# Optimization experiments

Hardware: AMD Instinct MI355X
Metric: run time of the kernel (lower is better)

Reference implementation:

```python
import jax, jax.numpy as jnp
import numpy as np

TOP_K = 2


def setup_inputs() -> dict:
    key = jax.random.key(0)
    ks = jax.random.split(key, 5)
    B, S, H, E, F = 2, 4096, 2048, 8, 4096
    scale_h = 1.0 / np.sqrt(H)
    scale_f = 1.0 / np.sqrt(F)
    return {
        "hidden_states": jax.random.normal(ks[0], (B, S, H), jnp.float32),
        "gate_w": jax.random.normal(ks[1], (E, H), jnp.float32) * scale_h,
        "w1": jax.random.normal(ks[2], (E, F, H), jnp.float32) * scale_h,
        "w3": jax.random.normal(ks[3], (E, F, H), jnp.float32) * scale_h,
        "w2": jax.random.normal(ks[4], (E, H, F), jnp.float32) * scale_f,
    }


def reference(hidden_states, gate_w, w1, w3, w2):
    B, S, H = hidden_states.shape
    E = gate_w.shape[0]
    x = hidden_states.reshape(-1, H)                      # [T, H]
    T = x.shape[0]

    # Router: logits -> softmax(fp32) -> top-k -> renormalize
    router_logits = x @ gate_w.T                          # [T, E]
    probs = jax.nn.softmax(router_logits.astype(jnp.float32), axis=-1)
    topk_w, topk_idx = jax.lax.top_k(probs, TOP_K)        # [T, k]
    topk_w = topk_w / jnp.sum(topk_w, axis=-1, keepdims=True)
    topk_w = topk_w.astype(x.dtype)

    # Per-expert combine weight (0 for unselected experts) [T, E]
    combine = jnp.sum(jax.nn.one_hot(topk_idx, E, dtype=x.dtype)
                      * topk_w[..., None], axis=1)

    # Expert SwiGLU MLPs, weighted-accumulated (loop over fixed E=8)
    out = jnp.zeros((T, H), dtype=x.dtype)
    for e in range(E):
        h = jax.nn.silu(x @ w1[e].T) * (x @ w3[e].T)      # [T, F]
        out = out + (h @ w2[e].T) * combine[:, e:e + 1]   # [T, H]

    return out.reshape(B, S, H), router_logits
```

## Files before the change

### kernel.cpp

```cpp
#include <hip/hip_runtime.h>
#include <math.h>

#define T_TOK 8192
#define H_DIM 2048
#define F_DIM 4096
#define E_NUM 8
#define MAXPAIR (T_TOK * 2)
#define MAX_MT 136
#define BM 128
#define BN 128
#define BK 32
#define NCONV 2048

typedef __attribute__((ext_vector_type(4))) float f32x4;
typedef __attribute__((ext_vector_type(8))) short s16x8;
typedef __attribute__((ext_vector_type(8))) __bf16 bf16x8;
typedef __attribute__((ext_vector_type(4))) unsigned short u16x4;

__device__ __forceinline__ unsigned short f2bf(float f) {
  unsigned int u = __float_as_uint(f);
  u += 0x7FFFu + ((u >> 16) & 1u);
  return (unsigned short)(u >> 16);
}

__device__ __forceinline__ s16x8 pack8(f32x4 a, f32x4 b) {
  s16x8 r;
  r[0] = (short)f2bf(a.x); r[1] = (short)f2bf(a.y);
  r[2] = (short)f2bf(a.z); r[3] = (short)f2bf(a.w);
  r[4] = (short)f2bf(b.x); r[5] = (short)f2bf(b.y);
  r[6] = (short)f2bf(b.z); r[7] = (short)f2bf(b.w);
  return r;
}

#define GLD16(gsrc, ldst)                                                      \
  __builtin_amdgcn_global_load_lds(                                            \
      (__attribute__((address_space(1))) void*)(gsrc),                         \
      (__attribute__((address_space(3))) void*)(ldst), 16, 0, 0)

__global__ __launch_bounds__(256) void convert_kernel(
    const float* __restrict__ src, unsigned short* __restrict__ dst,
    long long n8) {
  long long i = (long long)blockIdx.x * 256 + threadIdx.x;
  const long long stride = (long long)gridDim.x * 256;
  for (; i < n8; i += stride) {
    f32x4 a = *(const f32x4*)(src + i * 8);
    f32x4 b = *(const f32x4*)(src + i * 8 + 4);
    *(s16x8*)(dst + i * 8) = pack8(a, b);
  }
}

__global__ __launch_bounds__(256) void router_kernel(
    const float* __restrict__ x, const float* __restrict__ gw,
    float* __restrict__ logits, unsigned short* __restrict__ xb,
    int* __restrict__ ctrl, int* __restrict__ tIdx, float* __restrict__ tW) {
  const int wid = threadIdx.x >> 6, lane = threadIdx.x & 63;
  const int t = blockIdx.x * 4 + wid;
  const float* xr = x + (size_t)t * H_DIM;
  float acc[E_NUM];
#pragma unroll
  for (int e = 0; e < E_NUM; ++e) acc[e] = 0.f;
#pragma unroll
  for (int c = 0; c < H_DIM / 256; ++c) {
    const int h0 = c * 256 + lane * 4;
    f32x4 xv = *(const f32x4*)(xr + h0);
    u16x4 p;
    p.x = f2bf(xv.x); p.y = f2bf(xv.y); p.z = f2bf(xv.z); p.w = f2bf(xv.w);
    *(u16x4*)(xb + (size_t)t * H_DIM + h0) = p;
#pragma unroll
    for (int e = 0; e < E_NUM; ++e) {
      f32x4 gv = *(const f32x4*)(gw + (size_t)e * H_DIM + h0);
      acc[e] += xv.x * gv.x + xv.y * gv.y + xv.z * gv.z + xv.w * gv.w;
    }
  }
#pragma unroll
  for (int e = 0; e < E_NUM; ++e) {
#pragma unroll
    for (int off = 32; off >= 1; off >>= 1) acc[e] += __shfl_xor(acc[e], off, 64);
  }
  if (lane == 0) {
#pragma unroll
    for (int e = 0; e < E_NUM; ++e) logits[(size_t)t * E_NUM + e] = acc[e];
    int i0 = 0;
    float m0 = acc[0];
    for (int e = 1; e < E_NUM; ++e)
      if (acc[e] > m0) { m0 = acc[e]; i0 = e; }
    int i1 = -1;
    float m1 = -3.4e38f;
    for (int e = 0; e < E_NUM; ++e)
      if (e != i0 && acc[e] > m1) { m1 = acc[e]; i1 = e; }
    float ex = expf(m1 - m0);
    float w0 = 1.f / (1.f + ex);
    float w1 = ex * w0;
    tIdx[t * 2] = i0; tIdx[t * 2 + 1] = i1;
    tW[t * 2] = w0;  tW[t * 2 + 1] = w1;
    atomicAdd(&ctrl[i0], 1);
    atomicAdd(&ctrl[i1], 1);
  }
}

__global__ __launch_bounds__(256) void plan_kernel(int* __restrict__ ctrl) {
  __shared__ int cnt[E_NUM], offs[E_NUM + 1], tbase[E_NUM + 1];
  const int t = threadIdx.x;
  if (t < E_NUM) cnt[t] = ctrl[t];
  __syncthreads();
  if (t == 0) {
    int off = 0, mt = 0;
    for (int e = 0; e < E_NUM; ++e) {
      offs[e] = off; tbase[e] = mt;
      ctrl[8 + e] = off;
      ctrl[16 + e] = off;
      off += cnt[e];
      mt += (cnt[e] + BM - 1) / BM;
    }
    offs[E_NUM] = off; tbase[E_NUM] = mt;
    ctrl[24] = mt;
  }
  __syncthreads();
  const int total = tbase[E_NUM];
  for (int i = t; i < total; i += 256) {
    int e = 0;
    while (tbase[e + 1] <= i) ++e;
    ctrl[32 + i] = e;
    ctrl[32 + MAX_MT + i] = offs[e] + (i - tbase[e]) * BM;
  }
}

__global__ __launch_bounds__(256) void scatter_kernel(
    const int* __restrict__ tIdx, const float* __restrict__ tW,
    int* __restrict__ ctrl, int* __restrict__ pairTok,
    float* __restrict__ pairWgt) {
  const int t = blockIdx.x * 256 + threadIdx.x;
  if (t >= T_TOK) return;
#pragma unroll
  for (int j = 0; j < 2; ++j) {
    const int e = tIdx[t * 2 + j];
    const int pos = atomicAdd(&ctrl[16 + e], 1);
    pairTok[pos] = t;
    pairWgt[pos] = tW[t * 2 + j];
  }
}

template <int BBF>
__global__ __launch_bounds__(256, 2) void gemm1_kernel(
    const float* __restrict__ w1f, const float* __restrict__ w3f,
    const unsigned short* __restrict__ w1b,
    const unsigned short* __restrict__ w3b,
    const unsigned short* __restrict__ xb, const int* __restrict__ ctrl,
    const int* __restrict__ pairTok, unsigned short* __restrict__ hbuf,
    const float* __restrict__ w2f, unsigned short* __restrict__ w2b,
    int nconv) {
  int gid = blockIdx.x;
  const int nconv3 = nconv * 3;
  if (gid < nconv3) {
    if ((gid % 3) == 2) {
      const int cid = gid / 3;
      const long long per = (long long)E_NUM * F_DIM * H_DIM / 8 / NCONV;
      long long i = (long long)cid * per + threadIdx.x;
      const long long end = (long long)(cid + 1) * per;
      for (; i < end; i += 256) {
        f32x4 a = *(const f32x4*)(w2f + i * 8);
        f32x4 b = *(const f32x4*)(w2f + i * 8 + 4);
        *(s16x8*)(w2b + i * 8) = pack8(a, b);
      }
      return;
    }
    gid = gid - (gid + 1) / 3;
  } else {
    gid = gid - nconv;
  }

  const int mtTotal = ctrl[24];
  const int mt = gid >> 5;
  const int nt = gid & 31;
  if (mt >= mtTotal) return;
  const int e = ctrl[32 + mt];
  const int mbase = ctrl[32 + MAX_MT + mt];
  int mValid = ctrl[8 + e] + ctrl[e] - mbase;
  if (mValid > BM) mValid = BM;
  const int nbase = nt * BN;

  __shared__ __align__(16) short sA[3][BM * BK];
  __shared__ __align__(16) short sB1[3][BM * BK];
  __shared__ __align__(16) short sB3[3][BM * BK];
  __shared__ int sTok[BM];

  const int tid = threadIdx.x;
  if (tid < BM) sTok[tid] = pairTok[mbase + (tid < mValid ? tid : 0)];
  __syncthreads();

  const int c0 = tid, c1 = tid + 256;
  const int r0 = c0 >> 2, r1 = c1 >> 2;
  const int kg0 = (c0 & 3) ^ ((r0 >> 1) & 3);
  const int kg1 = (c1 & 3) ^ ((r1 >> 1) & 3);

  const unsigned short* srcA0 = xb + (size_t)sTok[r0] * H_DIM + kg0 * 8;
  const unsigned short* srcA1 = xb + (size_t)sTok[r1] * H_DIM + kg1 * 8;
  const size_t wbase = (size_t)e * F_DIM * H_DIM;
  const float *f10, *f11, *f30, *f31;
  const unsigned short *p10, *p11, *p30, *p31;
  if constexpr (BBF) {
    p10 = w1b + wbase + (size_t)(nbase + r0) * H_DIM + kg0 * 8;
    p11 = w1b + wbase + (size_t)(nbase + r1) * H_DIM + kg1 * 8;
    p30 = w3b + wbase + (size_t)(nbase + r0) * H_DIM + kg0 * 8;
    p31 = w3b + wbase + (size_t)(nbase + r1) * H_DIM + kg1 * 8;
  } else {
    f10 = w1f + wbase + (size_t)(nbase + r0) * H_DIM + kg0 * 8;
    f11 = w1f + wbase + (size_t)(nbase + r1) * H_DIM + kg1 * 8;
    f30 = w3f + wbase + (size_t)(nbase + r0) * H_DIM + kg0 * 8;
    f31 = w3f + wbase + (size_t)(nbase + r1) * H_DIM + kg1 * 8;
  }

  f32x4 acc1[4][4], acc3[4][4];
  const f32x4 fz = {0.f, 0.f, 0.f, 0.f};
#pragma unroll
  for (int i = 0; i < 4; ++i)
#pragma unroll
    for (int j = 0; j < 4; ++j) { acc1[i][j] = fz; acc3[i][j] = fz; }

  const int lane = tid & 63, wid = tid >> 6;
  const int wm = (wid >> 1) * 64, wn = (wid & 1) * 64;
  const int rl = lane & 15, kq = lane >> 4;

  int aIdx[4], bIdx[4];
#pragma unroll
  for (int i = 0; i < 4; ++i) {
    const int ra = wm + i * 16 + rl;
    aIdx[i] = ra * BK + ((kq ^ ((ra >> 1) & 3)) * 8);
    const int rb = wn + i * 16 + rl;
    bIdx[i] = rb * BK + ((kq ^ ((rb >> 1) & 3)) * 8);
  }

#define STAGE1(buf, k0)                                                        \
  {                                                                            \
    GLD16(srcA0 + (k0), &sA[buf][c0 * 8]);                                     \
    GLD16(srcA1 + (k0), &sA[buf][c1 * 8]);                                     \
    if constexpr (BBF) {                                                       \
      GLD16(p10 + (k0), &sB1[buf][c0 * 8]);                                    \
      GLD16(p11 + (k0), &sB1[buf][c1 * 8]);                                    \
      GLD16(p30 + (k0), &sB3[buf][c0 * 8]);                                    \
      GLD16(p31 + (k0), &sB3[buf][c1 * 8]);                                    \
    } else {                                                                   \
      f32x4 t0 = *(const f32x4*)(f10 + (k0));                                  \
      f32x4 t1 = *(const f32x4*)(f10 + (k0) + 4);                              \
      *(s16x8*)&sB1[buf][c0 * 8] = pack8(t0, t1);                              \
      t0 = *(const f32x4*)(f11 + (k0));                                        \
      t1 = *(const f32x4*)(f11 + (k0) + 4);                                    \
      *(s16x8*)&sB1[buf][c1 * 8] = pack8(t0, t1);                              \
      t0 = *(const f32x4*)(f30 + (k0));                                        \
      t1 = *(const f32x4*)(f30 + (k0) + 4);                                    \
      *(s16x8*)&sB3[buf][c0 * 8] = pack8(t0, t1);                              \
      t0 = *(const f32x4*)(f31 + (k0));                                        \
      t1 = *(const f32x4*)(f31 + (k0) + 4);                                    \
      *(s16x8*)&sB3[buf][c1 * 8] = pack8(t0, t1);                              \
    }                                                                          \
  }

  STAGE1(0, 0);
  STAGE1(1, BK);

  const int NS = H_DIM / BK;
  int cur = 0;
  for (int s = 0; s < NS; ++s) {
    if (s + 2 < NS) {
      const int nxt = (cur + 2 >= 3) ? cur - 1 : cur + 2;
      STAGE1(nxt, (s + 2) * BK);
      if constexpr (BBF)
        asm volatile("s_waitcnt vmcnt(12)" ::: "memory");
      else
        asm volatile("s_waitcnt vmcnt(0) lgkmcnt(0)" ::: "memory");
    } else if (s + 2 == NS) {
      if constexpr (BBF)
        asm volatile("s_waitcnt vmcnt(6)" ::: "memory");
      else
        asm volatile("s_waitcnt vmcnt(0) lgkmcnt(0)" ::: "memory");
    } else {
      asm volatile("s_waitcnt vmcnt(0) lgkmcnt(0)" ::: "memory");
    }
    __builtin_amdgcn_s_barrier();
    asm volatile("" ::: "memory");

    bf16x8 af[4], bf1[4], bf3[4];
#pragma unroll
    for (int i = 0; i < 4; ++i) {
      af[i] = *(const bf16x8*)&sA[cur][aIdx[i]];
      bf1[i] = *(const bf16x8*)&sB1[cur][bIdx[i]];
      bf3[i] = *(const bf16x8*)&sB3[cur][bIdx[i]];
    }
    __builtin_amdgcn_s_setprio(1);
#pragma unroll
    for (int mr = 0; mr < 4; ++mr)
#pragma unroll
      for (int nr = 0; nr < 4; ++nr) {
        acc1[mr][nr] = __builtin_amdgcn_mfma_f32_16x16x32_bf16(
            af[mr], bf1[nr], acc1[mr][nr], 0, 0, 0);
        acc3[mr][nr] = __builtin_amdgcn_mfma_f32_16x16x32_bf16(
            af[mr], bf3[nr], acc3[mr][nr], 0, 0, 0);
      }
    __builtin_amdgcn_s_setprio(0);
    asm volatile("" ::: "memory");
    __builtin_amdgcn_s_barrier();
    cur = (cur + 1 >= 3) ? 0 : cur + 1;
  }

#pragma unroll
  for (int mr = 0; mr < 4; ++mr) {
#pragma unroll
    for (int j = 0; j < 4; ++j) {
      const int row = wm + mr * 16 + kq * 4 + j;
      if (row < mValid) {
        unsigned short* dst =
            hbuf + (size_t)(mbase + row) * F_DIM + nbase + wn + rl;
#pragma unroll
        for (int nr = 0; nr < 4; ++nr) {
          const float z = acc1[mr][nr][j];
          const float hv = (z / (1.f + expf(-z))) * acc3[mr][nr][j];
          dst[nr * 16] = f2bf(hv);
        }
      }
    }
  }
#undef STAGE1
}

template <int BBF>
__global__ __launch_bounds__(256, 2) void gemm2_kernel(
    const float* __restrict__ w2f, const unsigned short* __restrict__ w2b,
    const unsigned short* __restrict__ hbuf, const int* __restrict__ ctrl,
    const int* __restrict__ pairTok, const float* __restrict__ pairWgt,
    float* __restrict__ out) {
  const int mtTotal = ctrl[24];
  const int mt = blockIdx.x >> 4;
  const int nt = blockIdx.x & 15;
  if (mt >= mtTotal) return;
  const int e = ctrl[32 + mt];
  const int mbase = ctrl[32 + MAX_MT + mt];
  int mValid = ctrl[8 + e] + ctrl[e] - mbase;
  if (mValid > BM) mValid = BM;
  const int nbase = nt * BN;

  __shared__ __align__(16) short sA[3][BM * BK];
  __shared__ __align__(16) short sB[3][BM * BK];
  __shared__ int sTok[BM];
  __shared__ float sWgt[BM];

  const int tid = threadIdx.x;
  if (tid < BM) {
    const int p = mbase + (tid < mValid ? tid : 0);
    sTok[tid] = pairTok[p];
    sWgt[tid] = pairWgt[p];
  }
  __syncthreads();

  const int c0 = tid, c1 = tid + 256;
  const int r0 = c0 >> 2, r1 = c1 >> 2;
  const int kg0 = (c0 & 3) ^ ((r0 >> 1) & 3);
  const int kg1 = (c1 & 3) ^ ((r1 >> 1) & 3);

  size_t pa0 = (size_t)(mbase + r0); if (pa0 > MAXPAIR - 1) pa0 = MAXPAIR - 1;
  size_t pa1 = (size_t)(mbase + r1); if (pa1 > MAXPAIR - 1) pa1 = MAXPAIR - 1;
  const unsigned short* srcA0 = hbuf + pa0 * F_DIM + kg0 * 8;
  const unsigned short* srcA1 = hbuf + pa1 * F_DIM + kg1 * 8;
  const size_t wbase = (size_t)e * H_DIM * F_DIM;
  const float *fw0, *fw1;
  const unsigned short *pw0, *pw1;
  if constexpr (BBF) {
    pw0 = w2b + wbase + (size_t)(nbase + r0) * F_DIM + kg0 * 8;
    pw1 = w2b + wbase + (size_t)(nbase + r1) * F_DIM + kg1 * 8;
  } else {
    fw0 = w2f + wbase + (size_t)(nbase + r0) * F_DIM + kg0 * 8;
    fw1 = w2f + wbase + (size_t)(nbase + r1) * F_DIM + kg1 * 8;
  }

  f32x4 acc[4][4];
  const f32x4 fz = {0.f, 0.f, 0.f, 0.f};
#pragma unroll
  for (int i = 0; i < 4; ++i)
#pragma unroll
    for (int j = 0; j < 4; ++j) acc[i][j] = fz;

  const int lane = tid & 63, wid = tid >> 6;
  const int wm = (wid >> 1) * 64, wn = (wid & 1) * 64;
  const int rl = lane & 15, kq = lane >> 4;

  int aIdx[4], bIdx[4];
#pragma unroll
  for (int i = 0; i < 4; ++i) {
    const int ra = wm + i * 16 + rl;
    aIdx[i] = ra * BK + ((kq ^ ((ra >> 1) & 3)) * 8);
    const int rb = wn + i * 16 + rl;
    bIdx[i] = rb * BK + ((kq ^ ((rb >> 1) & 3)) * 8);
  }

#define STAGE2(buf, k0)                                                        \
  {                                                                            \
    GLD16(srcA0 + (k0), &sA[buf][c0 * 8]);                                     \
    GLD16(srcA1 + (k0), &sA[buf][c1 * 8]);                                     \
    if constexpr (BBF) {                                                       \
      GLD16(pw0 + (k0), &sB[buf][c0 * 8]);                                     \
      GLD16(pw1 + (k0), &sB[buf][c1 * 8]);                                     \
    } else {                                                                   \
      f32x4 t0 = *(const f32x4*)(fw0 + (k0));                                  \
      f32x4 t1 = *(const f32x4*)(fw0 + (k0) + 4);                              \
      *(s16x8*)&sB[buf][c0 * 8] = pack8(t0, t1);                               \
      t0 = *(const f32x4*)(fw1 + (k0));                                        \
      t1 = *(const f32x4*)(fw1 + (k0) + 4);                                    \
      *(s16x8*)&sB[buf][c1 * 8] = pack8(t0, t1);                               \
    }                                                                          \
  }

  STAGE2(0, 0);
  STAGE2(1, BK);

  const int NS = F_DIM / BK;
  int cur = 0;
  for (int s = 0; s < NS; ++s) {
    if (s + 2 < NS) {
      const int nxt = (cur + 2 >= 3) ? cur - 1 : cur + 2;
      STAGE2(nxt, (s + 2) * BK);
      if constexpr (BBF)
        asm volatile("s_waitcnt vmcnt(8)" ::: "memory");
      else
        asm volatile("s_waitcnt vmcnt(0) lgkmcnt(0)" ::: "memory");
    } else if (s + 2 == NS) {
      if constexpr (BBF)
        asm volatile("s_waitcnt vmcnt(4)" ::: "memory");
      else
        asm volatile("s_waitcnt vmcnt(0) lgkmcnt(0)" ::: "memory");
    } else {
      asm volatile("s_waitcnt vmcnt(0) lgkmcnt(0)" ::: "memory");
    }
    __builtin_amdgcn_s_barrier();
    asm volatile("" ::: "memory");

    bf16x8 af[4], bf[4];
#pragma unroll
    for (int i = 0; i < 4; ++i) {
      af[i] = *(const bf16x8*)&sA[cur][aIdx[i]];
      bf[i] = *(const bf16x8*)&sB[cur][bIdx[i]];
    }
    __builtin_amdgcn_s_setprio(1);
#pragma unroll
    for (int mr = 0; mr < 4; ++mr)
#pragma unroll
      for (int nr = 0; nr < 4; ++nr)
        acc[mr][nr] = __builtin_amdgcn_mfma_f32_16x16x32_bf16(
            af[mr], bf[nr], acc[mr][nr], 0, 0, 0);
    __builtin_amdgcn_s_setprio(0);
    asm volatile("" ::: "memory");
    __builtin_amdgcn_s_barrier();
    cur = (cur + 1 >= 3) ? 0 : cur + 1;
  }

#pragma unroll
  for (int mr = 0; mr < 4; ++mr) {
#pragma unroll
    for (int j = 0; j < 4; ++j) {
      const int row = wm + mr * 16 + kq * 4 + j;
      if (row < mValid) {
        const int tok = sTok[row];
        const float w = sWgt[row];
        float* dst = out + (size_t)tok * H_DIM + nbase + wn + rl;
#pragma unroll
        for (int nr = 0; nr < 4; ++nr)
          unsafeAtomicAdd(dst + nr * 16, w * acc[mr][nr][j]);
      }
    }
  }
#undef STAGE2
}

extern "C" void kernel_launch(void* const* d_in, const int* in_sizes, int n_in,
                              void* d_out, int out_size, void* d_ws,
                              size_t ws_size, hipStream_t stream) {
  const float* x  = (const float*)d_in[0];
  const float* gw = (const float*)d_in[1];
  const float* w1 = (const float*)d_in[2];
  const float* w3 = (const float*)d_in[3];
  const float* w2 = (const float*)d_in[4];
  float* out = (float*)d_out;
  float* logits = out + (size_t)T_TOK * H_DIM;

  char* ws = (char*)d_ws;
  const size_t HDR = 1u << 20;
  const size_t XB_SZ = (size_t)T_TOK * H_DIM * 2;
  const size_t HB_SZ = (size_t)MAXPAIR * F_DIM * 2;
  const size_t W_SZ  = (size_t)E_NUM * F_DIM * H_DIM * 2;

  int* ctrl = (int*)(ws);
  int* tIdx = (int*)(ws + 4096);
  float* tW = (float*)(ws + 4096 + 65536);
  int* pairTok = (int*)(ws + 4096 + 131072);
  float* pairWgt = (float*)(ws + 4096 + 196608);
  unsigned short* xb = (unsigned short*)(ws + HDR);
  unsigned short* hbuf = (unsigned short*)(ws + HDR + XB_SZ);
  unsigned short* w1b = (unsigned short*)(ws + HDR + XB_SZ + HB_SZ);
  unsigned short* w3b = w1b + W_SZ / 2;
  unsigned short* w2b = w3b + W_SZ / 2;

  const bool cw13 = ws_size >= HDR + XB_SZ + HB_SZ + 2 * W_SZ;
  const bool cw2  = ws_size >= HDR + XB_SZ + HB_SZ + 3 * W_SZ;

  hipMemsetAsync(ctrl, 0, 4096, stream);
  hipMemsetAsync(out, 0, (size_t)T_TOK * H_DIM * sizeof(float), stream);

  const long long N8 = (long long)E_NUM * F_DIM * H_DIM / 8;
  if (cw13) {
    convert_kernel<<<2048, 256, 0, stream>>>(w1, w1b, N8);
    convert_kernel<<<2048, 256, 0, stream>>>(w3, w3b, N8);
  }

  router_kernel<<<T_TOK / 4, 256, 0, stream>>>(x, gw, logits, xb, ctrl, tIdx, tW);
  plan_kernel<<<1, 256, 0, stream>>>(ctrl);
  scatter_kernel<<<T_TOK / 256, 256, 0, stream>>>(tIdx, tW, ctrl, pairTok, pairWgt);

  const int NG = MAX_MT * 32;
  if (cw13) {
    const int nconv = cw2 ? NCONV : 0;
    gemm1_kernel<1><<<NG + nconv, 256, 0, stream>>>(
        w1, w3, w1b, w3b, xb, ctrl, pairTok, hbuf, w2, w2b, nconv);
  } else {
    gemm1_kernel<0><<<NG, 256, 0, stream>>>(
        w1, w3, w1b, w3b, xb, ctrl, pairTok, hbuf, w2, w2b, 0);
  }
  if (cw2)
    gemm2_kernel<1><<<MAX_MT * 16, 256, 0, stream>>>(w2, w2b, hbuf, ctrl,
                                                     pairTok, pairWgt, out);
  else
    gemm2_kernel<0><<<MAX_MT * 16, 256, 0, stream>>>(w2, w2b, hbuf, ctrl,
                                                     pairTok, pairWgt, out);
}
```

Baseline: 1.548 ms.

## Drop separate w1/w3 bf16 conversion; convert fp32 weights inline in gemm1 pipeline

Removes the two standalone convert kernels that turned w1 and w3 into bf16 in workspace. gemm1 now always loads fp32 weights into registers, converts them with native bf16 casts, and writes them into double-buffered LDS, staggering the w1 and w3 loads around the two MFMA phases to hide latency. This avoids writing and re-reading the converted weight copies, at the cost of fetching twice the bytes per weight tile inside the GEMM and having only two stages of buffering instead of three.

Result: slower. 1.689 ms (+9.1%).

```diff
diff --git a/kernel.cpp b/kernel.cpp
--- a/kernel.cpp
+++ b/kernel.cpp
@@ -32,22 +32,19 @@
   return r;
 }
 
+__device__ __forceinline__ s16x8 pack8c(f32x4 a, f32x4 b) {
+  union { bf16x8 h; s16x8 s; } u;
+  u.h[0] = (__bf16)a.x; u.h[1] = (__bf16)a.y;
+  u.h[2] = (__bf16)a.z; u.h[3] = (__bf16)a.w;
+  u.h[4] = (__bf16)b.x; u.h[5] = (__bf16)b.y;
+  u.h[6] = (__bf16)b.z; u.h[7] = (__bf16)b.w;
+  return u.s;
+}
+
 #define GLD16(gsrc, ldst)                                                      \
   __builtin_amdgcn_global_load_lds(                                            \
       (__attribute__((address_space(1))) void*)(gsrc),                         \
       (__attribute__((address_space(3))) void*)(ldst), 16, 0, 0)
-
-__global__ __launch_bounds__(256) void convert_kernel(
-    const float* __restrict__ src, unsigned short* __restrict__ dst,
-    long long n8) {
-  long long i = (long long)blockIdx.x * 256 + threadIdx.x;
-  const long long stride = (long long)gridDim.x * 256;
-  for (; i < n8; i += stride) {
-    f32x4 a = *(const f32x4*)(src + i * 8);
-    f32x4 b = *(const f32x4*)(src + i * 8 + 4);
-    *(s16x8*)(dst + i * 8) = pack8(a, b);
-  }
-}
 
 __global__ __launch_bounds__(256) void router_kernel(
     const float* __restrict__ x, const float* __restrict__ gw,
@@ -140,11 +137,8 @@
   }
 }
 
-template <int BBF>
 __global__ __launch_bounds__(256, 2) void gemm1_kernel(
     const float* __restrict__ w1f, const float* __restrict__ w3f,
-    const unsigned short* __restrict__ w1b,
-    const unsigned short* __restrict__ w3b,
     const unsigned short* __restrict__ xb, const int* __restrict__ ctrl,
     const int* __restrict__ pairTok, unsigned short* __restrict__ hbuf,
     const float* __restrict__ w2f, unsigned short* __restrict__ w2b,
@@ -179,9 +173,9 @@
   if (mValid > BM) mValid = BM;
   const int nbase = nt * BN;
 
-  __shared__ __align__(16) short sA[3][BM * BK];
-  __shared__ __align__(16) short sB1[3][BM * BK];
-  __shared__ __align__(16) short sB3[3][BM * BK];
+  __shared__ __align__(16) short sA[2][BM * BK];
+  __shared__ __align__(16) short sB1[2][BM * BK];
+  __shared__ __align__(16) short sB3[2][BM * BK];
   __shared__ int sTok[BM];
 
   const int tid = threadIdx.x;
@@ -196,19 +190,10 @@
   const unsigned short* srcA0 = xb + (size_t)sTok[r0] * H_DIM + kg0 * 8;
   const unsigned short* srcA1 = xb + (size_t)sTok[r1] * H_DIM + kg1 * 8;
   const size_t wbase = (size_t)e * F_DIM * H_DIM;
-  const float *f10, *f11, *f30, *f31;
-  const unsigned short *p10, *p11, *p30, *p31;
-  if constexpr (BBF) {
-    p10 = w1b + wbase + (size_t)(nbase + r0) * H_DIM + kg0 * 8;
-    p11 = w1b + wbase + (size_t)(nbase + r1) * H_DIM + kg1 * 8;
-    p30 = w3b + wbase + (size_t)(nbase + r0) * H_DIM + kg0 * 8;
-    p31 = w3b + wbase + (size_t)(nbase + r1) * H_DIM + kg1 * 8;
-  } else {
-    f10 = w1f + wbase + (size_t)(nbase + r0) * H_DIM + kg0 * 8;
-    f11 = w1f + wbase + (size_t)(nbase + r1) * H_DIM + kg1 * 8;
-    f30 = w3f + wbase + (size_t)(nbase + r0) * H_DIM + kg0 * 8;
-    f31 = w3f + wbase + (size_t)(nbase + r1) * H_DIM + kg1 * 8;
-  }
+  const float* f10 = w1f + wbase + (size_t)(nbase + r0) * H_DIM + kg0 * 8;
+  const float* f11 = w1f + wbase + (size_t)(nbase + r1) * H_DIM + kg1 * 8;
+  const float* f30 = w3f + wbase + (size_t)(nbase + r0) * H_DIM + kg0 * 8;
+  const float* f31 = w3f + wbase + (size_t)(nbase + r1) * H_DIM + kg1 * 8;
 
   f32x4 acc1[4][4], acc3[4][4];
   const f32x4 fz = {0.f, 0.f, 0.f, 0.f};
@@ -230,76 +215,95 @@
     bIdx[i] = rb * BK + ((kq ^ ((rb >> 1) & 3)) * 8);
   }
 
-#define STAGE1(buf, k0)                                                        \
+  f32x4 b1r[4], b3r[4];
+
+#define ISSUE_B1(k0)                                                           \
+  {                                                                            \
+    b1r[0] = *(const f32x4*)(f10 + (k0));                                      \
+    b1r[1] = *(const f32x4*)(f10 + (k0) + 4);                                  \
+    b1r[2] = *(const f32x4*)(f11 + (k0));                                      \
+    b1r[3] = *(const f32x4*)(f11 + (k0) + 4);                                  \
+  }
+#define ISSUE_B3(k0)                                                           \
+  {                                                                            \
+    b3r[0] = *(const f32x4*)(f30 + (k0));                                      \
+    b3r[1] = *(const f32x4*)(f30 + (k0) + 4);                                  \
+    b3r[2] = *(const f32x4*)(f31 + (k0));                                      \
+    b3r[3] = *(const f32x4*)(f31 + (k0) + 4);                                  \
+  }
+#define ISSUE_A(buf, k0)                                                       \
   {                                                                            \
     GLD16(srcA0 + (k0), &sA[buf][c0 * 8]);                                     \
     GLD16(srcA1 + (k0), &sA[buf][c1 * 8]);                                     \
-    if constexpr (BBF) {                                                       \
-      GLD16(p10 + (k0), &sB1[buf][c0 * 8]);                                    \
-      GLD16(p11 + (k0), &sB1[buf][c1 * 8]);                                    \
-      GLD16(p30 + (k0), &sB3[buf][c0 * 8]);                                    \
-      GLD16(p31 + (k0), &sB3[buf][c1 * 8]);                                    \
-    } else {                                                                   \
-      f32x4 t0 = *(const f32x4*)(f10 + (k0));                                  \
-      f32x4 t1 = *(const f32x4*)(f10 + (k0) + 4);                              \
-      *(s16x8*)&sB1[buf][c0 * 8] = pack8(t0, t1);                              \
-      t0 = *(const f32x4*)(f11 + (k0));                                        \
-      t1 = *(const f32x4*)(f11 + (k0) + 4);                                    \
-      *(s16x8*)&sB1[buf][c1 * 8] = pack8(t0, t1);                              \
-      t0 = *(const f32x4*)(f30 + (k0));                                        \
-      t1 = *(const f32x4*)(f30 + (k0) + 4);                                    \
-      *(s16x8*)&sB3[buf][c0 * 8] = pack8(t0, t1);                              \
-      t0 = *(const f32x4*)(f31 + (k0));                                        \
-      t1 = *(const f32x4*)(f31 + (k0) + 4);                                    \
-      *(s16x8*)&sB3[buf][c1 * 8] = pack8(t0, t1);                              \
-    }                                                                          \
-  }
-
-  STAGE1(0, 0);
-  STAGE1(1, BK);
+  }
+#define WRITE_B1(buf)                                                          \
+  {                                                                            \
+    *(s16x8*)&sB1[buf][c0 * 8] = pack8c(b1r[0], b1r[1]);                       \
+    *(s16x8*)&sB1[buf][c1 * 8] = pack8c(b1r[2], b1r[3]);                       \
+  }
+#define WRITE_B3(buf)                                                          \
+  {                                                                            \
+    *(s16x8*)&sB3[buf][c0 * 8] = pack8c(b3r[0], b3r[1]);                       \
+    *(s16x8*)&sB3[buf][c1 * 8] = pack8c(b3r[2], b3r[3]);                       \
+  }
+
+  ISSUE_B1(0);
+  ISSUE_A(0, 0);
+  ISSUE_B3(0);
+  asm volatile("" ::: "memory");
+  WRITE_B1(0);
+  WRITE_B3(0);
+  asm volatile("s_waitcnt vmcnt(0) lgkmcnt(0)" ::: "memory");
+  __builtin_amdgcn_s_barrier();
 
   const int NS = H_DIM / BK;
-  int cur = 0;
+#pragma unroll 2
   for (int s = 0; s < NS; ++s) {
-    if (s + 2 < NS) {
-      const int nxt = (cur + 2 >= 3) ? cur - 1 : cur + 2;
-      STAGE1(nxt, (s + 2) * BK);
-      if constexpr (BBF)
-        asm volatile("s_waitcnt vmcnt(12)" ::: "memory");
-      else
-        asm volatile("s_waitcnt vmcnt(0) lgkmcnt(0)" ::: "memory");
-    } else if (s + 2 == NS) {
-      if constexpr (BBF)
-        asm volatile("s_waitcnt vmcnt(6)" ::: "memory");
-      else
-        asm volatile("s_waitcnt vmcnt(0) lgkmcnt(0)" ::: "memory");
-    } else {
-      asm volatile("s_waitcnt vmcnt(0) lgkmcnt(0)" ::: "memory");
-    }
-    __builtin_amdgcn_s_barrier();
+    const int cur = s & 1, nxt = cur ^ 1;
+    const int kn = (s + 1) * BK;
+    const bool more = (s + 1 < NS);
+    if (more) {
+      ISSUE_B1(kn);
+      ISSUE_A(nxt, kn);
+    }
     asm volatile("" ::: "memory");
 
-    bf16x8 af[4], bf1[4], bf3[4];
+    bf16x8 af[4], bf1[4];
 #pragma unroll
     for (int i = 0; i < 4; ++i) {
       af[i] = *(const bf16x8*)&sA[cur][aIdx[i]];
       bf1[i] = *(const bf16x8*)&sB1[cur][bIdx[i]];
-      bf3[i] = *(const bf16x8*)&sB3[cur][bIdx[i]];
     }
     __builtin_amdgcn_s_setprio(1);
 #pragma unroll
     for (int mr = 0; mr < 4; ++mr)
 #pragma unroll
-      for (int nr = 0; nr < 4; ++nr) {
+      for (int nr = 0; nr < 4; ++nr)
         acc1[mr][nr] = __builtin_amdgcn_mfma_f32_16x16x32_bf16(
             af[mr], bf1[nr], acc1[mr][nr], 0, 0, 0);
+    __builtin_amdgcn_s_setprio(0);
+
+    if (more) {
+      ISSUE_B3(kn);
+      asm volatile("" ::: "memory");
+      WRITE_B1(nxt);
+    }
+
+    bf16x8 bf3[4];
+#pragma unroll
+    for (int i = 0; i < 4; ++i) bf3[i] = *(const bf16x8*)&sB3[cur][bIdx[i]];
+    __builtin_amdgcn_s_setprio(1);
+#pragma unroll
+    for (int mr = 0; mr < 4; ++mr)
+#pragma unroll
+      for (int nr = 0; nr < 4; ++nr)
         acc3[mr][nr] = __builtin_amdgcn_mfma_f32_16x16x32_bf16(
             af[mr], bf3[nr], acc3[mr][nr], 0, 0, 0);
-      }
     __builtin_amdgcn_s_setprio(0);
-    asm volatile("" ::: "memory");
+
+    if (more) WRITE_B3(nxt);
+    asm volatile("s_waitcnt vmcnt(0) lgkmcnt(0)" ::: "memory");
     __builtin_amdgcn_s_barrier();
-    cur = (cur + 1 >= 3) ? 0 : cur + 1;
   }
 
 #pragma unroll
@@ -319,7 +323,11 @@
       }
     }
   }
-#undef STAGE1
+#undef ISSUE_B1
+#undef ISSUE_B3
+#undef ISSUE_A
+#undef WRITE_B1
+#undef WRITE_B3
 }
 
 template <int BBF>
@@ -493,35 +501,22 @@
   float* pairWgt = (float*)(ws + 4096 + 196608);
   unsigned short* xb = (unsigned short*)(ws + HDR);
   unsigned short* hbuf = (unsigned short*)(ws + HDR + XB_SZ);
-  unsigned short* w1b = (unsigned short*)(ws + HDR + XB_SZ + HB_SZ);
-  unsigned short* w3b = w1b + W_SZ / 2;
-  unsigned short* w2b = w3b + W_SZ / 2;
-
-  const bool cw13 = ws_size >= HDR + XB_SZ + HB_SZ + 2 * W_SZ;
-  const bool cw2  = ws_size >= HDR + XB_SZ + HB_SZ + 3 * W_SZ;
+  unsigned short* w2b = (unsigned short*)(ws + HDR + XB_SZ + HB_SZ);
+
+  const bool cw2 = ws_size >= HDR + XB_SZ + HB_SZ + W_SZ;
 
   hipMemsetAsync(ctrl, 0, 4096, stream);
   hipMemsetAsync(out, 0, (size_t)T_TOK * H_DIM * sizeof(float), stream);
-
-  const long long N8 = (long long)E_NUM * F_DIM * H_DIM / 8;
-  if (cw13) {
-    convert_kernel<<<2048, 256, 0, stream>>>(w1, w1b, N8);
-    convert_kernel<<<2048, 256, 0, stream>>>(w3, w3b, N8);
-  }
 
   router_kernel<<<T_TOK / 4, 256, 0, stream>>>(x, gw, logits, xb, ctrl, tIdx, tW);
   plan_kernel<<<1, 256, 0, stream>>>(ctrl);
   scatter_kernel<<<T_TOK / 256, 256, 0, stream>>>(tIdx, tW, ctrl, pairTok, pairWgt);
 
   const int NG = MAX_MT * 32;
-  if (cw13) {
-    const int nconv = cw2 ? NCONV : 0;
-    gemm1_kernel<1><<<NG + nconv, 256, 0, stream>>>(
-        w1, w3, w1b, w3b, xb, ctrl, pairTok, hbuf, w2, w2b, nconv);
-  } else {
-    gemm1_kernel<0><<<NG, 256, 0, stream>>>(
-        w1, w3, w1b, w3b, xb, ctrl, pairTok, hbuf, w2, w2b, 0);
-  }
+  const int nconv = cw2 ? NCONV : 0;
+  gemm1_kernel<<<NG + nconv * 3 - (cw2 ? NCONV * 2 : 0), 256, 0, stream>>>(
+      w1, w3, xb, ctrl, pairTok, hbuf, w2, w2b, nconv);
+
   if (cw2)
     gemm2_kernel<1><<<MAX_MT * 16, 256, 0, stream>>>(w2, w2b, hbuf, ctrl,
                                                      pairTok, pairWgt, out);
```

## Convert w1/w3 to bf16 lazily inside gemm1 with per-tile claim flags

Applied to the files above, without the earlier changes.

Drops the two standalone fp32-to-bf16 conversion kernels for w1 and w3. Inside gemm1, the first block that needs a given (expert, N-tile) weight slab claims it with an atomic CAS, converts that slab to bf16, and publishes a flag. Other blocks spin-wait on the flag before reading. This overlaps the conversion with the GEMM and skips converting unused slabs. The cost is spin-waits on the critical path, and a possible deadlock if the claiming block is not resident while others wait.

Result: slower. 5.083 ms (+228.4%).

```diff
diff --git a/kernel.cpp b/kernel.cpp
--- a/kernel.cpp
+++ b/kernel.cpp
@@ -36,18 +36,6 @@
   __builtin_amdgcn_global_load_lds(                                            \
       (__attribute__((address_space(1))) void*)(gsrc),                         \
       (__attribute__((address_space(3))) void*)(ldst), 16, 0, 0)
-
-__global__ __launch_bounds__(256) void convert_kernel(
-    const float* __restrict__ src, unsigned short* __restrict__ dst,
-    long long n8) {
-  long long i = (long long)blockIdx.x * 256 + threadIdx.x;
-  const long long stride = (long long)gridDim.x * 256;
-  for (; i < n8; i += stride) {
-    f32x4 a = *(const f32x4*)(src + i * 8);
-    f32x4 b = *(const f32x4*)(src + i * 8 + 4);
-    *(s16x8*)(dst + i * 8) = pack8(a, b);
-  }
-}
 
 __global__ __launch_bounds__(256) void router_kernel(
     const float* __restrict__ x, const float* __restrict__ gw,
@@ -143,12 +131,11 @@
 template <int BBF>
 __global__ __launch_bounds__(256, 2) void gemm1_kernel(
     const float* __restrict__ w1f, const float* __restrict__ w3f,
-    const unsigned short* __restrict__ w1b,
-    const unsigned short* __restrict__ w3b,
+    unsigned short* __restrict__ w1b, unsigned short* __restrict__ w3b,
     const unsigned short* __restrict__ xb, const int* __restrict__ ctrl,
-    const int* __restrict__ pairTok, unsigned short* __restrict__ hbuf,
-    const float* __restrict__ w2f, unsigned short* __restrict__ w2b,
-    int nconv) {
+    int* __restrict__ flags, const int* __restrict__ pairTok,
+    unsigned short* __restrict__ hbuf, const float* __restrict__ w2f,
+    unsigned short* __restrict__ w2b, int nconv) {
   int gid = blockIdx.x;
   const int nconv3 = nconv * 3;
   if (gid < nconv3) {
@@ -183,9 +170,53 @@
   __shared__ __align__(16) short sB1[3][BM * BK];
   __shared__ __align__(16) short sB3[3][BM * BK];
   __shared__ int sTok[BM];
+  __shared__ int sClaim;
 
   const int tid = threadIdx.x;
   if (tid < BM) sTok[tid] = pairTok[mbase + (tid < mValid ? tid : 0)];
+
+  const size_t wbase = (size_t)e * F_DIM * H_DIM;
+
+  if constexpr (BBF) {
+    int* flag = flags + e * 32 + nt;
+    if (tid == 0) {
+      int cur = __hip_atomic_load(flag, __ATOMIC_ACQUIRE,
+                                  __HIP_MEMORY_SCOPE_AGENT);
+      int mine = 0;
+      if (cur == 0) {
+        int exp = 0;
+        mine = __hip_atomic_compare_exchange_strong(
+            flag, &exp, 1, __ATOMIC_ACQ_REL, __ATOMIC_ACQUIRE,
+            __HIP_MEMORY_SCOPE_AGENT);
+      }
+      sClaim = mine;
+    }
+    __syncthreads();
+    if (sClaim) {
+      const size_t pb = wbase + (size_t)nbase * H_DIM;
+      const int NPE = BM * H_DIM / 8;
+      for (int i = tid; i < NPE; i += 256) {
+        f32x4 a = *(const f32x4*)(w1f + pb + (size_t)i * 8);
+        f32x4 b = *(const f32x4*)(w1f + pb + (size_t)i * 8 + 4);
+        *(s16x8*)(w1b + pb + (size_t)i * 8) = pack8(a, b);
+        a = *(const f32x4*)(w3f + pb + (size_t)i * 8);
+        b = *(const f32x4*)(w3f + pb + (size_t)i * 8 + 4);
+        *(s16x8*)(w3b + pb + (size_t)i * 8) = pack8(a, b);
+      }
+      __syncthreads();
+      if (tid == 0) {
+        __threadfence();
+        __hip_atomic_store(flag, 2, __ATOMIC_RELEASE,
+                           __HIP_MEMORY_SCOPE_AGENT);
+      }
+    } else {
+      if (tid == 0) {
+        while (__hip_atomic_load(flag, __ATOMIC_ACQUIRE,
+                                 __HIP_MEMORY_SCOPE_AGENT) != 2)
+          __builtin_amdgcn_s_sleep(8);
+      }
+    }
+  }
   __syncthreads();
 
   const int c0 = tid, c1 = tid + 256;
@@ -195,7 +226,6 @@
 
   const unsigned short* srcA0 = xb + (size_t)sTok[r0] * H_DIM + kg0 * 8;
   const unsigned short* srcA1 = xb + (size_t)sTok[r1] * H_DIM + kg1 * 8;
-  const size_t wbase = (size_t)e * F_DIM * H_DIM;
   const float *f10, *f11, *f30, *f31;
   const unsigned short *p10, *p11, *p30, *p31;
   if constexpr (BBF) {
@@ -503,12 +533,6 @@
   hipMemsetAsync(ctrl, 0, 4096, stream);
   hipMemsetAsync(out, 0, (size_t)T_TOK * H_DIM * sizeof(float), stream);
 
-  const long long N8 = (long long)E_NUM * F_DIM * H_DIM / 8;
-  if (cw13) {
-    convert_kernel<<<2048, 256, 0, stream>>>(w1, w1b, N8);
-    convert_kernel<<<2048, 256, 0, stream>>>(w3, w3b, N8);
-  }
-
   router_kernel<<<T_TOK / 4, 256, 0, stream>>>(x, gw, logits, xb, ctrl, tIdx, tW);
   plan_kernel<<<1, 256, 0, stream>>>(ctrl);
   scatter_kernel<<<T_TOK / 256, 256, 0, stream>>>(tIdx, tW, ctrl, pairTok, pairWgt);
@@ -517,10 +541,10 @@
   if (cw13) {
     const int nconv = cw2 ? NCONV : 0;
     gemm1_kernel<1><<<NG + nconv, 256, 0, stream>>>(
-        w1, w3, w1b, w3b, xb, ctrl, pairTok, hbuf, w2, w2b, nconv);
+        w1, w3, w1b, w3b, xb, ctrl, ctrl + 512, pairTok, hbuf, w2, w2b, nconv);
   } else {
     gemm1_kernel<0><<<NG, 256, 0, stream>>>(
-        w1, w3, w1b, w3b, xb, ctrl, pairTok, hbuf, w2, w2b, 0);
+        w1, w3, w1b, w3b, xb, ctrl, ctrl + 512, pairTok, hbuf, w2, w2b, 0);
   }
   if (cw2)
     gemm2_kernel<1><<<MAX_MT * 16, 256, 0, stream>>>(w2, w2b, hbuf, ctrl,
```

## Widen gemm2 N tile to 256 and merge w1/w3 conversion launches

Applied to the files above, without the earlier changes.

The down-projection GEMM now uses a 128x256 output tile. Each wave computes 64x128 with 32 accumulators, so each block loads the A (hbuf) tile once for twice as many output columns, and the grid is halved. The w1 and w3 fp32-to-bf16 conversions are fused into a single launch covering both arrays. The wider tile raises register and LDS use, which may lower occupancy under the launch_bounds(256,2) hint, and it leaves fewer blocks to spread across CUs.

Measured after the change: 1.633 ms. 1.05x slower.

```diff
diff --git a/kernel.cpp b/kernel.cpp
--- a/kernel.cpp
+++ b/kernel.cpp
@@ -10,6 +10,7 @@
 #define BM 128
 #define BN 128
 #define BK 32
+#define BN2 256
 #define NCONV 2048
 
 typedef __attribute__((ext_vector_type(4))) float f32x4;
@@ -37,11 +38,16 @@
       (__attribute__((address_space(1))) void*)(gsrc),                         \
       (__attribute__((address_space(3))) void*)(ldst), 16, 0, 0)
 
-__global__ __launch_bounds__(256) void convert_kernel(
-    const float* __restrict__ src, unsigned short* __restrict__ dst,
+__global__ __launch_bounds__(256) void convert2_kernel(
+    const float* __restrict__ s1, unsigned short* __restrict__ d1,
+    const float* __restrict__ s2, unsigned short* __restrict__ d2,
     long long n8) {
-  long long i = (long long)blockIdx.x * 256 + threadIdx.x;
-  const long long stride = (long long)gridDim.x * 256;
+  const int half = gridDim.x / 2;
+  const float* src = (blockIdx.x < half) ? s1 : s2;
+  unsigned short* dst = (blockIdx.x < half) ? d1 : d2;
+  const int bid = (blockIdx.x < half) ? blockIdx.x : blockIdx.x - half;
+  long long i = (long long)bid * 256 + threadIdx.x;
+  const long long stride = (long long)half * 256;
   for (; i < n8; i += stride) {
     f32x4 a = *(const f32x4*)(src + i * 8);
     f32x4 b = *(const f32x4*)(src + i * 8 + 4);
@@ -329,17 +335,17 @@
     const int* __restrict__ pairTok, const float* __restrict__ pairWgt,
     float* __restrict__ out) {
   const int mtTotal = ctrl[24];
-  const int mt = blockIdx.x >> 4;
-  const int nt = blockIdx.x & 15;
+  const int mt = blockIdx.x >> 3;
+  const int nt = blockIdx.x & 7;
   if (mt >= mtTotal) return;
   const int e = ctrl[32 + mt];
   const int mbase = ctrl[32 + MAX_MT + mt];
   int mValid = ctrl[8 + e] + ctrl[e] - mbase;
   if (mValid > BM) mValid = BM;
-  const int nbase = nt * BN;
+  const int nbase = nt * BN2;
 
   __shared__ __align__(16) short sA[3][BM * BK];
-  __shared__ __align__(16) short sB[3][BM * BK];
+  __shared__ __align__(16) short sB[3][BN2 * BK];
   __shared__ int sTok[BM];
   __shared__ float sWgt[BM];
 
@@ -361,32 +367,39 @@
   const unsigned short* srcA0 = hbuf + pa0 * F_DIM + kg0 * 8;
   const unsigned short* srcA1 = hbuf + pa1 * F_DIM + kg1 * 8;
   const size_t wbase = (size_t)e * H_DIM * F_DIM;
-  const float *fw0, *fw1;
-  const unsigned short *pw0, *pw1;
-  if constexpr (BBF) {
-    pw0 = w2b + wbase + (size_t)(nbase + r0) * F_DIM + kg0 * 8;
-    pw1 = w2b + wbase + (size_t)(nbase + r1) * F_DIM + kg1 * 8;
-  } else {
-    fw0 = w2f + wbase + (size_t)(nbase + r0) * F_DIM + kg0 * 8;
-    fw1 = w2f + wbase + (size_t)(nbase + r1) * F_DIM + kg1 * 8;
-  }
-
-  f32x4 acc[4][4];
+
+  const float* fw[4];
+  const unsigned short* pw[4];
+#pragma unroll
+  for (int j = 0; j < 4; ++j) {
+    const int c = tid + j * 256;
+    const int row = c >> 2;
+    const int kg = (c & 3) ^ ((row >> 1) & 3);
+    if constexpr (BBF)
+      pw[j] = w2b + wbase + (size_t)(nbase + row) * F_DIM + kg * 8;
+    else
+      fw[j] = w2f + wbase + (size_t)(nbase + row) * F_DIM + kg * 8;
+  }
+
+  f32x4 acc[4][8];
   const f32x4 fz = {0.f, 0.f, 0.f, 0.f};
 #pragma unroll
   for (int i = 0; i < 4; ++i)
 #pragma unroll
-    for (int j = 0; j < 4; ++j) acc[i][j] = fz;
+    for (int j = 0; j < 8; ++j) acc[i][j] = fz;
 
   const int lane = tid & 63, wid = tid >> 6;
-  const int wm = (wid >> 1) * 64, wn = (wid & 1) * 64;
+  const int wm = (wid >> 1) * 64, wn = (wid & 1) * 128;
   const int rl = lane & 15, kq = lane >> 4;
 
-  int aIdx[4], bIdx[4];
+  int aIdx[4], bIdx[8];
 #pragma unroll
   for (int i = 0; i < 4; ++i) {
     const int ra = wm + i * 16 + rl;
     aIdx[i] = ra * BK + ((kq ^ ((ra >> 1) & 3)) * 8);
+  }
+#pragma unroll
+  for (int i = 0; i < 8; ++i) {
     const int rb = wn + i * 16 + rl;
     bIdx[i] = rb * BK + ((kq ^ ((rb >> 1) & 3)) * 8);
   }
@@ -396,15 +409,14 @@
     GLD16(srcA0 + (k0), &sA[buf][c0 * 8]);                                     \
     GLD16(srcA1 + (k0), &sA[buf][c1 * 8]);                                     \
     if constexpr (BBF) {                                                       \
-      GLD16(pw0 + (k0), &sB[buf][c0 * 8]);                                     \
-      GLD16(pw1 + (k0), &sB[buf][c1 * 8]);                                     \
+      _Pragma("unroll") for (int j = 0; j < 4; ++j)                            \
+          GLD16(pw[j] + (k0), &sB[buf][(tid + j * 256) * 8]);                  \
     } else {                                                                   \
-      f32x4 t0 = *(const f32x4*)(fw0 + (k0));                                  \
-      f32x4 t1 = *(const f32x4*)(fw0 + (k0) + 4);                              \
-      *(s16x8*)&sB[buf][c0 * 8] = pack8(t0, t1);                               \
-      t0 = *(const f32x4*)(fw1 + (k0));                                        \
-      t1 = *(const f32x4*)(fw1 + (k0) + 4);                                    \
-      *(s16x8*)&sB[buf][c1 * 8] = pack8(t0, t1);                               \
+      _Pragma("unroll") for (int j = 0; j < 4; ++j) {                          \
+        f32x4 t0 = *(const f32x4*)(fw[j] + (k0));                              \
+        f32x4 t1 = *(const f32x4*)(fw[j] + (k0) + 4);                          \
+        *(s16x8*)&sB[buf][(tid + j * 256) * 8] = pack8(t0, t1);                \
+      }                                                                        \
     }                                                                          \
   }
 
@@ -418,12 +430,12 @@
       const int nxt = (cur + 2 >= 3) ? cur - 1 : cur + 2;
       STAGE2(nxt, (s + 2) * BK);
       if constexpr (BBF)
-        asm volatile("s_waitcnt vmcnt(8)" ::: "memory");
+        asm volatile("s_waitcnt vmcnt(12)" ::: "memory");
       else
         asm volatile("s_waitcnt vmcnt(0) lgkmcnt(0)" ::: "memory");
     } else if (s + 2 == NS) {
       if constexpr (BBF)
-        asm volatile("s_waitcnt vmcnt(4)" ::: "memory");
+        asm volatile("s_waitcnt vmcnt(6)" ::: "memory");
       else
         asm volatile("s_waitcnt vmcnt(0) lgkmcnt(0)" ::: "memory");
     } else {
@@ -432,17 +444,16 @@
     __builtin_amdgcn_s_barrier();
     asm volatile("" ::: "memory");
 
-    bf16x8 af[4], bf[4];
-#pragma unroll
-    for (int i = 0; i < 4; ++i) {
-      af[i] = *(const bf16x8*)&sA[cur][aIdx[i]];
-      bf[i] = *(const bf16x8*)&sB[cur][bIdx[i]];
-    }
+    bf16x8 af[4], bf[8];
+#pragma unroll
+    for (int i = 0; i < 4; ++i) af[i] = *(const bf16x8*)&sA[cur][aIdx[i]];
+#pragma unroll
+    for (int i = 0; i < 8; ++i) bf[i] = *(const bf16x8*)&sB[cur][bIdx[i]];
     __builtin_amdgcn_s_setprio(1);
 #pragma unroll
     for (int mr = 0; mr < 4; ++mr)
 #pragma unroll
-      for (int nr = 0; nr < 4; ++nr)
+      for (int nr = 0; nr < 8; ++nr)
         acc[mr][nr] = __builtin_amdgcn_mfma_f32_16x16x32_bf16(
             af[mr], bf[nr], acc[mr][nr], 0, 0, 0);
     __builtin_amdgcn_s_setprio(0);
@@ -461,7 +472,7 @@
         const float w = sWgt[row];
         float* dst = out + (size_t)tok * H_DIM + nbase + wn + rl;
 #pragma unroll
-        for (int nr = 0; nr < 4; ++nr)
+        for (int nr = 0; nr < 8; ++nr)
           unsafeAtomicAdd(dst + nr * 16, w * acc[mr][nr][j]);
       }
     }
@@ -504,10 +515,8 @@
   hipMemsetAsync(out, 0, (size_t)T_TOK * H_DIM * sizeof(float), stream);
 
   const long long N8 = (long long)E_NUM * F_DIM * H_DIM / 8;
-  if (cw13) {
-    convert_kernel<<<2048, 256, 0, stream>>>(w1, w1b, N8);
-    convert_kernel<<<2048, 256, 0, stream>>>(w3, w3b, N8);
-  }
+  if (cw13)
+    convert2_kernel<<<4096, 256, 0, stream>>>(w1, w1b, w3, w3b, N8);
 
   router_kernel<<<T_TOK / 4, 256, 0, stream>>>(x, gw, logits, xb, ctrl, tIdx, tW);
   plan_kernel<<<1, 256, 0, stream>>>(ctrl);
@@ -523,9 +532,9 @@
         w1, w3, w1b, w3b, xb, ctrl, pairTok, hbuf, w2, w2b, 0);
   }
   if (cw2)
-    gemm2_kernel<1><<<MAX_MT * 16, 256, 0, stream>>>(w2, w2b, hbuf, ctrl,
-                                                     pairTok, pairWgt, out);
+    gemm2_kernel<1><<<MAX_MT * 8, 256, 0, stream>>>(w2, w2b, hbuf, ctrl,
+                                                    pairTok, pairWgt, out);
   else
-    gemm2_kernel<0><<<MAX_MT * 16, 256, 0, stream>>>(w2, w2b, hbuf, ctrl,
-                                                     pairTok, pairWgt, out);
-}
+    gemm2_kernel<0><<<MAX_MT * 8, 256, 0, stream>>>(w2, w2b, hbuf, ctrl,
+                                                    pairTok, pairWgt, out);
+}
```
